# Kernel tuning notes

Measured on AMD Instinct MI355X. Metric: run time of the kernel, lower is better.

## Reference

```python
import jax, jax.numpy as jnp
import numpy as np

EMBED_DIM = 1024
NUM_HEADS = 16
HEAD_DIM = EMBED_DIM // NUM_HEADS
SEG_LEN = 1024  # all segment_lengths equal, dilation_rate == 1


def setup_inputs() -> dict:
    key = jax.random.key(0)
    k1, k2, k3 = jax.random.split(key, 3)
    B, S, E = 2, 4096, EMBED_DIM
    x = jax.random.normal(k1, (B, S, E), dtype=jnp.float32)
    w_qkv = jax.random.normal(k2, (3 * E, E), dtype=jnp.float32) * (E ** -0.5)
    b_qkv = jnp.zeros((3 * E,), dtype=jnp.float32)
    w_out = jax.random.normal(k3, (E, E), dtype=jnp.float32) * (E ** -0.5)
    b_out = jnp.zeros((E,), dtype=jnp.float32)
    return {"x": x, "w_qkv": w_qkv, "b_qkv": b_qkv, "w_out": w_out, "b_out": b_out}


def reference(x, w_qkv, b_qkv, w_out, b_out):
    B, S, E = x.shape
    H, Dh = NUM_HEADS, HEAD_DIM
    scale = 1.0 / np.sqrt(Dh).astype(np.float32)
    # QKV projection
    qkv = x @ w_qkv.T + b_qkv                      # [B, S, 3E]
    qkv = qkv.reshape(B, S, 3, H, Dh).transpose(2, 0, 3, 1, 4)  # [3, B, H, S, Dh]
    q, k, v = qkv[0], qkv[1], qkv[2]
    # Segments tile the sequence; each query attends only within its segment
    # (block-diagonal attention; online-softmax combine across segments is
    # trivial since the segments are disjoint in the query dimension).
    n = S // SEG_LEN
    q = q.reshape(B, H, n, SEG_LEN, Dh)
    k = k.reshape(B, H, n, SEG_LEN, Dh)
    v = v.reshape(B, H, n, SEG_LEN, Dh)
    scores = jnp.einsum("bhnqd,bhnkd->bhnqk", q, k) * scale
    attn = jax.nn.softmax(scores, axis=-1)
    out = jnp.einsum("bhnqk,bhnkd->bhnqd", attn, v)  # [B, H, n, seg, Dh]
    out = out.reshape(B, H, S, Dh).transpose(0, 2, 1, 3).reshape(B, S, E)
    return out @ w_out.T + b_out
```

## Files before the change

kernel.cpp:

```cpp
#include <hip/hip_runtime.h>

typedef __bf16 bf16x8 __attribute__((ext_vector_type(8)));
typedef float f32x4 __attribute__((ext_vector_type(4)));

#define SL2E 0.18033688011112042f

__device__ __forceinline__ unsigned short f2bf(float f) {
  union { float f; unsigned u; } v; v.f = f;
  unsigned r = v.u + 0x7fffu + ((v.u >> 16) & 1u);
  return (unsigned short)(r >> 16);
}

__device__ __forceinline__ float fast_exp2(float x) {
#if __has_builtin(__builtin_amdgcn_exp2f)
  return __builtin_amdgcn_exp2f(x);
#else
  return exp2f(x);
#endif
}

__device__ __forceinline__ unsigned pack_bf2(float lo, float hi) {
  union { float f; unsigned u; } a, b;
  a.f = lo; b.f = hi;
#if __has_builtin(__builtin_amdgcn_perm)
  return __builtin_amdgcn_perm(b.u + 0x7fffu, a.u + 0x7fffu, 0x07060302u);
#else
  return ((b.u + 0x7fffu) & 0xffff0000u) | ((a.u + 0x7fffu) >> 16);
#endif
}

__global__ void f32_to_bf16_k(const float* __restrict__ in, unsigned short* __restrict__ out, int n4) {
  int i = blockIdx.x * blockDim.x + threadIdx.x;
  if (i >= n4) return;
  float4 v = ((const float4*)in)[i];
  ushort4 o;
  o.x = f2bf(v.x); o.y = f2bf(v.y); o.z = f2bf(v.z); o.w = f2bf(v.w);
  ((ushort4*)out)[i] = o;
}

__global__ __launch_bounds__(256) void gemm_qkv(
    const unsigned short* __restrict__ A,
    const unsigned short* __restrict__ Bt,
    const float* __restrict__ bias,
    unsigned short* __restrict__ Qb,
    unsigned short* __restrict__ Kb,
    unsigned short* __restrict__ Vtb) {
  const int K = 1024;
  __shared__ unsigned short As[128 * 40];
  __shared__ unsigned short Bs[128 * 40];
  int tid = threadIdx.x;
  int m0 = blockIdx.x * 128, n0 = blockIdx.y * 128;
  int w = tid >> 6, lane = tid & 63, l15 = lane & 15, quad = lane >> 4;
  int wm = (w & 1) * 64, wn = (w >> 1) * 64;

  f32x4 acc[4][4] = {};

  int c0 = tid, c1 = tid + 256;
  int ra0 = c0 >> 2, ca0 = (c0 & 3) * 8;
  int ra1 = c1 >> 2, ca1 = (c1 & 3) * 8;

  for (int kt = 0; kt < K; kt += 32) {
    __syncthreads();
    uint4 a0 = *(const uint4*)(A + (m0 + ra0) * K + kt + ca0);
    uint4 a1 = *(const uint4*)(A + (m0 + ra1) * K + kt + ca1);
    uint4 b0 = *(const uint4*)(Bt + (n0 + ra0) * K + kt + ca0);
    uint4 b1 = *(const uint4*)(Bt + (n0 + ra1) * K + kt + ca1);
    *(uint4*)(As + ra0 * 40 + ca0) = a0;
    *(uint4*)(As + ra1 * 40 + ca1) = a1;
    *(uint4*)(Bs + ra0 * 40 + ca0) = b0;
    *(uint4*)(Bs + ra1 * 40 + ca1) = b1;
    __syncthreads();
    bf16x8 af[4], bfr[4];
#pragma unroll
    for (int i = 0; i < 4; ++i) af[i] = *(const bf16x8*)(As + (wm + i * 16 + l15) * 40 + quad * 8);
#pragma unroll
    for (int j = 0; j < 4; ++j) bfr[j] = *(const bf16x8*)(Bs + (wn + j * 16 + l15) * 40 + quad * 8);
#pragma unroll
    for (int i = 0; i < 4; ++i)
#pragma unroll
      for (int j = 0; j < 4; ++j)
        acc[i][j] = __builtin_amdgcn_mfma_f32_16x16x32_bf16(af[i], bfr[j], acc[i][j], 0, 0, 0);
  }

  int b = m0 >> 12;
  int sblk = (m0 & 4095) + wm + quad * 4;
#pragma unroll
  for (int j = 0; j < 4; ++j) {
    int n_j = n0 + wn + j * 16 + l15;
    float bv = bias[n_j];
    int t = n_j >> 10, h = (n_j >> 6) & 15, d = n_j & 63;
    if (t == 2) {
      int vbase = ((b * 16 + h) * 64 + d) * 4096;
#pragma unroll
      for (int i = 0; i < 4; ++i) {
        int s = sblk + i * 16;
        ushort4 pk;
        pk.x = f2bf(acc[i][j][0] + bv);
        pk.y = f2bf(acc[i][j][1] + bv);
        pk.z = f2bf(acc[i][j][2] + bv);
        pk.w = f2bf(acc[i][j][3] + bv);
        *(ushort4*)(Vtb + vbase + s) = pk;
      }
    } else {
      unsigned short* dst = (t == 0) ? Qb : Kb;
      float sc = (t == 0) ? SL2E : 1.0f;
      int base = (b * 16 + h) * 4096 * 64 + d;
#pragma unroll
      for (int i = 0; i < 4; ++i)
#pragma unroll
        for (int r = 0; r < 4; ++r) {
          int s = sblk + i * 16 + r;
          dst[base + s * 64] = f2bf((acc[i][j][r] + bv) * sc);
        }
    }
  }
}

#define LDP 72

__global__ __launch_bounds__(256) void attn_k(
    const unsigned short* __restrict__ Qb,
    const unsigned short* __restrict__ Kb,
    const unsigned short* __restrict__ Vtb,
    unsigned short* __restrict__ Ab) {
  __shared__ unsigned short Ks[64 * LDP];
  __shared__ unsigned short Vs[64 * LDP];
  __shared__ unsigned short Ps[4][64 * LDP];

  int tid = threadIdx.x;
  int idx = blockIdx.x;
  int qblk = idx & 3, seg = (idx >> 2) & 3, h = (idx >> 4) & 15, b = idx >> 8;
  int w = tid >> 6, lane = tid & 63, l15 = lane & 15, quad = lane >> 4;
  int bh = b * 16 + h;
  int q0 = seg * 1024 + qblk * 256 + w * 64;

  const unsigned short* Qg = Qb + (bh * 4096 + q0) * 64;
  bf16x8 qf[4][2];
#pragma unroll
  for (int qb = 0; qb < 4; ++qb)
#pragma unroll
    for (int kk = 0; kk < 2; ++kk)
      qf[qb][kk] = *(const bf16x8*)(Qg + (qb * 16 + l15) * 64 + kk * 32 + quad * 8);

  bf16x8 ones;
#pragma unroll
  for (int i = 0; i < 8; ++i) ones[i] = (__bf16)1.0f;

  f32x4 o[4][4] = {};
  f32x4 lacc[4] = {};
  unsigned short* Pw = Ps[w];

  int sr = tid >> 3;
  int sc = (tid & 7) * 8;
  const unsigned short* Kg = Kb + (bh * 4096 + seg * 1024) * 64;
  const unsigned short* Vg = Vtb + bh * 64 * 4096 + seg * 1024;

  for (int kt = 0; kt < 16; ++kt) {
    int s0 = kt * 64;
    __syncthreads();
    *(uint4*)(Ks + sr * LDP + sc)        = *(const uint4*)(Kg + (s0 + sr) * 64 + sc);
    *(uint4*)(Ks + (sr + 32) * LDP + sc) = *(const uint4*)(Kg + (s0 + sr + 32) * 64 + sc);
    *(uint4*)(Vs + sr * LDP + sc)        = *(const uint4*)(Vg + sr * 4096 + s0 + sc);
    *(uint4*)(Vs + (sr + 32) * LDP + sc) = *(const uint4*)(Vg + (sr + 32) * 4096 + s0 + sc);
    __syncthreads();

#pragma unroll
    for (int half = 0; half < 2; ++half) {
      f32x4 st[2][4] = {};
#pragma unroll
      for (int kk = 0; kk < 2; ++kk) {
        bf16x8 kf0 = *(const bf16x8*)(Ks + (half * 32 + l15) * LDP + kk * 32 + quad * 8);
        bf16x8 kf1 = *(const bf16x8*)(Ks + (half * 32 + 16 + l15) * LDP + kk * 32 + quad * 8);
#pragma unroll
        for (int qb = 0; qb < 4; ++qb) {
          st[0][qb] = __builtin_amdgcn_mfma_f32_16x16x32_bf16(kf0, qf[qb][kk], st[0][qb], 0, 0, 0);
          st[1][qb] = __builtin_amdgcn_mfma_f32_16x16x32_bf16(kf1, qf[qb][kk], st[1][qb], 0, 0, 0);
        }
      }
#pragma unroll
      for (int kb = 0; kb < 2; ++kb)
#pragma unroll
        for (int qb = 0; qb < 4; ++qb) {
          f32x4 s = st[kb][qb];
          float p0 = fast_exp2(s[0]), p1 = fast_exp2(s[1]);
          float p2 = fast_exp2(s[2]), p3 = fast_exp2(s[3]);
          uint2 d;
          d.x = pack_bf2(p0, p1);
          d.y = pack_bf2(p2, p3);
          *(uint2*)(Pw + (qb * 16 + l15) * LDP + (half * 2 + kb) * 16 + quad * 4) = d;
        }
    }

#pragma unroll
    for (int kk = 0; kk < 2; ++kk) {
      bf16x8 vf[4];
#pragma unroll
      for (int db = 0; db < 4; ++db)
        vf[db] = *(const bf16x8*)(Vs + (db * 16 + l15) * LDP + kk * 32 + quad * 8);
#pragma unroll
      for (int qb = 0; qb < 4; ++qb) {
        bf16x8 pf = *(const bf16x8*)(Pw + (qb * 16 + l15) * LDP + kk * 32 + quad * 8);
        lacc[qb] = __builtin_amdgcn_mfma_f32_16x16x32_bf16(pf, ones, lacc[qb], 0, 0, 0);
#pragma unroll
        for (int db = 0; db < 4; ++db)
          o[qb][db] = __builtin_amdgcn_mfma_f32_16x16x32_bf16(pf, vf[db], o[qb][db], 0, 0, 0);
      }
    }
  }

#pragma unroll
  for (int qb = 0; qb < 4; ++qb)
#pragma unroll
    for (int r = 0; r < 4; ++r) {
      float inv = 1.0f / lacc[qb][r];
      int sg = q0 + qb * 16 + quad * 4 + r;
      int base = (b * 4096 + sg) * 1024 + h * 64;
#pragma unroll
      for (int db = 0; db < 4; ++db)
        Ab[base + db * 16 + l15] = f2bf(o[qb][db][r] * inv);
    }
}

__global__ __launch_bounds__(256) void gemm_out(
    const unsigned short* __restrict__ A,
    const unsigned short* __restrict__ Bt,
    const float* __restrict__ bias,
    float* __restrict__ C) {
  const int K = 1024;
  __shared__ unsigned short As[128 * 40];
  __shared__ unsigned short Bs[128 * 40];
  int tid = threadIdx.x;
  int m0 = blockIdx.x * 128, n0 = blockIdx.y * 128;
  int w = tid >> 6, lane = tid & 63, l15 = lane & 15, quad = lane >> 4;
  int wm = (w & 1) * 64, wn = (w >> 1) * 64;

  f32x4 acc[4][4] = {};

  int c0 = tid, c1 = tid + 256;
  int ra0 = c0 >> 2, ca0 = (c0 & 3) * 8;
  int ra1 = c1 >> 2, ca1 = (c1 & 3) * 8;

  for (int kt = 0; kt < K; kt += 32) {
    __syncthreads();
    uint4 a0 = *(const uint4*)(A + (m0 + ra0) * K + kt + ca0);
    uint4 a1 = *(const uint4*)(A + (m0 + ra1) * K + kt + ca1);
    uint4 b0 = *(const uint4*)(Bt + (n0 + ra0) * K + kt + ca0);
    uint4 b1 = *(const uint4*)(Bt + (n0 + ra1) * K + kt + ca1);
    *(uint4*)(As + ra0 * 40 + ca0) = a0;
    *(uint4*)(As + ra1 * 40 + ca1) = a1;
    *(uint4*)(Bs + ra0 * 40 + ca0) = b0;
    *(uint4*)(Bs + ra1 * 40 + ca1) = b1;
    __syncthreads();
    bf16x8 af[4], bfr[4];
#pragma unroll
    for (int i = 0; i < 4; ++i) af[i] = *(const bf16x8*)(As + (wm + i * 16 + l15) * 40 + quad * 8);
#pragma unroll
    for (int j = 0; j < 4; ++j) bfr[j] = *(const bf16x8*)(Bs + (wn + j * 16 + l15) * 40 + quad * 8);
#pragma unroll
    for (int i = 0; i < 4; ++i)
#pragma unroll
      for (int j = 0; j < 4; ++j)
        acc[i][j] = __builtin_amdgcn_mfma_f32_16x16x32_bf16(af[i], bfr[j], acc[i][j], 0, 0, 0);
  }

#pragma unroll
  for (int j = 0; j < 4; ++j) {
    int n_j = n0 + wn + j * 16 + l15;
    float bv = bias[n_j];
#pragma unroll
    for (int i = 0; i < 4; ++i)
#pragma unroll
      for (int r = 0; r < 4; ++r) {
        int m = m0 + wm + i * 16 + quad * 4 + r;
        C[m * 1024 + n_j] = acc[i][j][r] + bv;
      }
  }
}

extern "C" void kernel_launch(void* const* d_in, const int* in_sizes, int n_in,
                              void* d_out, int out_size, void* d_ws, size_t ws_size,
                              hipStream_t stream) {
  const float* x     = (const float*)d_in[0];
  const float* w_qkv = (const float*)d_in[1];
  const float* b_qkv = (const float*)d_in[2];
  const float* w_out = (const float*)d_in[3];
  const float* b_out = (const float*)d_in[4];
  float* out = (float*)d_out;
  char* ws = (char*)d_ws;

  unsigned short* wqkvb = (unsigned short*)(ws);
  unsigned short* woutb = (unsigned short*)(ws + 6291456);
  unsigned short* Qb    = (unsigned short*)(ws + 8388608);
  unsigned short* Kb    = (unsigned short*)(ws + 25165824);
  unsigned short* Vtb   = (unsigned short*)(ws + 41943040);
  unsigned short* xb    = (unsigned short*)(ws + 58720256);
  unsigned short* Ab    = xb;

  f32_to_bf16_k<<<8192, 256, 0, stream>>>(x, xb, 2097152);
  f32_to_bf16_k<<<3072, 256, 0, stream>>>(w_qkv, wqkvb, 786432);
  f32_to_bf16_k<<<1024, 256, 0, stream>>>(w_out, woutb, 262144);
  gemm_qkv<<<dim3(64, 24), 256, 0, stream>>>(xb, wqkvb, b_qkv, Qb, Kb, Vtb);
  attn_k<<<512, 256, 0, stream>>>(Qb, Kb, Vtb, Ab);
  gemm_out<<<dim3(64, 8), 256, 0, stream>>>(Ab, woutb, b_out, out);
}
```

Before: 266.8 us.

## Use direct global-to-LDS loads in GEMMs, shrink attention P buffer, fuse conversions

Merges the three fp32-to-bf16 conversion launches into one kernel. Both GEMMs now stage A/B tiles with global_load_lds straight into unpadded 32-wide LDS rows, skipping the register round trip. The attention kernel replaces the MFMA-with-ones row-sum with a scalar accumulation plus cross-lane shuffles. It also shrinks each wave's P staging buffer to 16 rows, written per query block, with a launch-bounds hint of 3 blocks per CU for higher occupancy. Risks are LDS bank conflicts from the unpadded layout and a row sum taken from fp32 probabilities rather than the bf16-rounded ones fed to the PV MFMA.

```diff
diff --git a/kernel.cpp b/kernel.cpp
--- a/kernel.cpp
+++ b/kernel.cpp
@@ -29,13 +29,25 @@
 #endif
 }
 
-__global__ void f32_to_bf16_k(const float* __restrict__ in, unsigned short* __restrict__ out, int n4) {
-  int i = blockIdx.x * blockDim.x + threadIdx.x;
-  if (i >= n4) return;
-  float4 v = ((const float4*)in)[i];
+__device__ __forceinline__ void gload16(const unsigned short* g, unsigned short* l) {
+  __builtin_amdgcn_global_load_lds(
+      (const __attribute__((address_space(1))) unsigned int*)g,
+      (__attribute__((address_space(3))) unsigned int*)l, 16, 0, 0);
+}
+
+__global__ __launch_bounds__(256) void f32_to_bf16_all(
+    const float* __restrict__ x, const float* __restrict__ wq, const float* __restrict__ wo,
+    unsigned short* __restrict__ xb, unsigned short* __restrict__ wqb, unsigned short* __restrict__ wob) {
+  int i = blockIdx.x * 256 + threadIdx.x;
+  const float* src; unsigned short* dst; int off;
+  if (i < 2097152) { src = x; dst = xb; off = i; }
+  else if (i < 2883584) { src = wq; dst = wqb; off = i - 2097152; }
+  else if (i < 3145728) { src = wo; dst = wob; off = i - 2883584; }
+  else return;
+  float4 v = ((const float4*)src)[off];
   ushort4 o;
   o.x = f2bf(v.x); o.y = f2bf(v.y); o.z = f2bf(v.z); o.w = f2bf(v.w);
-  ((ushort4*)out)[i] = o;
+  ((ushort4*)dst)[off] = o;
 }
 
 __global__ __launch_bounds__(256) void gemm_qkv(
@@ -46,8 +58,8 @@
     unsigned short* __restrict__ Kb,
     unsigned short* __restrict__ Vtb) {
   const int K = 1024;
-  __shared__ unsigned short As[128 * 40];
-  __shared__ unsigned short Bs[128 * 40];
+  __shared__ unsigned short As[128 * 32];
+  __shared__ unsigned short Bs[128 * 32];
   int tid = threadIdx.x;
   int m0 = blockIdx.x * 128, n0 = blockIdx.y * 128;
   int w = tid >> 6, lane = tid & 63, l15 = lane & 15, quad = lane >> 4;
@@ -55,26 +67,24 @@
 
   f32x4 acc[4][4] = {};
 
-  int c0 = tid, c1 = tid + 256;
-  int ra0 = c0 >> 2, ca0 = (c0 & 3) * 8;
-  int ra1 = c1 >> 2, ca1 = (c1 & 3) * 8;
+  int srow = lane >> 2, scol = (lane & 3) * 8;
+  const unsigned short* Ag0 = A + (m0 + w * 32 + srow) * K + scol;
+  const unsigned short* Bg0 = Bt + (n0 + w * 32 + srow) * K + scol;
+  unsigned short* Asl = As + w * 1024 + lane * 8;
+  unsigned short* Bsl = Bs + w * 1024 + lane * 8;
 
   for (int kt = 0; kt < K; kt += 32) {
     __syncthreads();
-    uint4 a0 = *(const uint4*)(A + (m0 + ra0) * K + kt + ca0);
-    uint4 a1 = *(const uint4*)(A + (m0 + ra1) * K + kt + ca1);
-    uint4 b0 = *(const uint4*)(Bt + (n0 + ra0) * K + kt + ca0);
-    uint4 b1 = *(const uint4*)(Bt + (n0 + ra1) * K + kt + ca1);
-    *(uint4*)(As + ra0 * 40 + ca0) = a0;
-    *(uint4*)(As + ra1 * 40 + ca1) = a1;
-    *(uint4*)(Bs + ra0 * 40 + ca0) = b0;
-    *(uint4*)(Bs + ra1 * 40 + ca1) = b1;
+    gload16(Ag0 + kt, Asl);
+    gload16(Ag0 + 16 * K + kt, Asl + 512);
+    gload16(Bg0 + kt, Bsl);
+    gload16(Bg0 + 16 * K + kt, Bsl + 512);
     __syncthreads();
     bf16x8 af[4], bfr[4];
 #pragma unroll
-    for (int i = 0; i < 4; ++i) af[i] = *(const bf16x8*)(As + (wm + i * 16 + l15) * 40 + quad * 8);
-#pragma unroll
-    for (int j = 0; j < 4; ++j) bfr[j] = *(const bf16x8*)(Bs + (wn + j * 16 + l15) * 40 + quad * 8);
+    for (int i = 0; i < 4; ++i) af[i] = *(const bf16x8*)(As + (wm + i * 16 + l15) * 32 + quad * 8);
+#pragma unroll
+    for (int j = 0; j < 4; ++j) bfr[j] = *(const bf16x8*)(Bs + (wn + j * 16 + l15) * 32 + quad * 8);
 #pragma unroll
     for (int i = 0; i < 4; ++i)
 #pragma unroll
@@ -118,14 +128,14 @@
 
 #define LDP 72
 
-__global__ __launch_bounds__(256) void attn_k(
+__global__ __launch_bounds__(256, 3) void attn_k(
     const unsigned short* __restrict__ Qb,
     const unsigned short* __restrict__ Kb,
     const unsigned short* __restrict__ Vtb,
     unsigned short* __restrict__ Ab) {
   __shared__ unsigned short Ks[64 * LDP];
   __shared__ unsigned short Vs[64 * LDP];
-  __shared__ unsigned short Ps[4][64 * LDP];
+  __shared__ unsigned short Ps[4][16 * LDP];
 
   int tid = threadIdx.x;
   int idx = blockIdx.x;
@@ -142,12 +152,8 @@
     for (int kk = 0; kk < 2; ++kk)
       qf[qb][kk] = *(const bf16x8*)(Qg + (qb * 16 + l15) * 64 + kk * 32 + quad * 8);
 
-  bf16x8 ones;
-#pragma unroll
-  for (int i = 0; i < 8; ++i) ones[i] = (__bf16)1.0f;
-
   f32x4 o[4][4] = {};
-  f32x4 lacc[4] = {};
+  float lsum[4] = {0.f, 0.f, 0.f, 0.f};
   unsigned short* Pw = Ps[w];
 
   int sr = tid >> 3;
@@ -164,6 +170,7 @@
     *(uint4*)(Vs + (sr + 32) * LDP + sc) = *(const uint4*)(Vg + (sr + 32) * 4096 + s0 + sc);
     __syncthreads();
 
+    uint2 pp[4][4];
 #pragma unroll
     for (int half = 0; half < 2; ++half) {
       f32x4 st[2][4] = {};
@@ -184,35 +191,50 @@
           f32x4 s = st[kb][qb];
           float p0 = fast_exp2(s[0]), p1 = fast_exp2(s[1]);
           float p2 = fast_exp2(s[2]), p3 = fast_exp2(s[3]);
+          lsum[qb] += (p0 + p1) + (p2 + p3);
           uint2 d;
           d.x = pack_bf2(p0, p1);
           d.y = pack_bf2(p2, p3);
-          *(uint2*)(Pw + (qb * 16 + l15) * LDP + (half * 2 + kb) * 16 + quad * 4) = d;
+          pp[qb][half * 2 + kb] = d;
         }
     }
 
-#pragma unroll
-    for (int kk = 0; kk < 2; ++kk) {
-      bf16x8 vf[4];
+    bf16x8 vf[2][4];
+#pragma unroll
+    for (int kk = 0; kk < 2; ++kk)
 #pragma unroll
       for (int db = 0; db < 4; ++db)
-        vf[db] = *(const bf16x8*)(Vs + (db * 16 + l15) * LDP + kk * 32 + quad * 8);
-#pragma unroll
-      for (int qb = 0; qb < 4; ++qb) {
-        bf16x8 pf = *(const bf16x8*)(Pw + (qb * 16 + l15) * LDP + kk * 32 + quad * 8);
-        lacc[qb] = __builtin_amdgcn_mfma_f32_16x16x32_bf16(pf, ones, lacc[qb], 0, 0, 0);
+        vf[kk][db] = *(const bf16x8*)(Vs + (db * 16 + l15) * LDP + kk * 32 + quad * 8);
+#pragma unroll
+    for (int qb = 0; qb < 4; ++qb) {
+#pragma unroll
+      for (int g = 0; g < 4; ++g)
+        *(uint2*)(Pw + l15 * LDP + g * 16 + quad * 4) = pp[qb][g];
+#pragma unroll
+      for (int kk = 0; kk < 2; ++kk) {
+        bf16x8 pa = *(const bf16x8*)(Pw + l15 * LDP + kk * 32 + quad * 8);
 #pragma unroll
         for (int db = 0; db < 4; ++db)
-          o[qb][db] = __builtin_amdgcn_mfma_f32_16x16x32_bf16(pf, vf[db], o[qb][db], 0, 0, 0);
+          o[qb][db] = __builtin_amdgcn_mfma_f32_16x16x32_bf16(pa, vf[kk][db], o[qb][db], 0, 0, 0);
       }
     }
   }
 
 #pragma unroll
+  for (int qb = 0; qb < 4; ++qb) {
+    lsum[qb] += __shfl_xor(lsum[qb], 16);
+    lsum[qb] += __shfl_xor(lsum[qb], 32);
+  }
+  float* Pf = (float*)Ps[w];
+  if (quad == 0) {
+#pragma unroll
+    for (int qb = 0; qb < 4; ++qb) Pf[qb * 16 + l15] = lsum[qb];
+  }
+#pragma unroll
   for (int qb = 0; qb < 4; ++qb)
 #pragma unroll
     for (int r = 0; r < 4; ++r) {
-      float inv = 1.0f / lacc[qb][r];
+      float inv = 1.0f / Pf[qb * 16 + quad * 4 + r];
       int sg = q0 + qb * 16 + quad * 4 + r;
       int base = (b * 4096 + sg) * 1024 + h * 64;
 #pragma unroll
@@ -227,8 +249,8 @@
     const float* __restrict__ bias,
     float* __restrict__ C) {
   const int K = 1024;
-  __shared__ unsigned short As[128 * 40];
-  __shared__ unsigned short Bs[128 * 40];
+  __shared__ unsigned short As[128 * 32];
+  __shared__ unsigned short Bs[128 * 32];
   int tid = threadIdx.x;
   int m0 = blockIdx.x * 128, n0 = blockIdx.y * 128;
   int w = tid >> 6, lane = tid & 63, l15 = lane & 15, quad = lane >> 4;
@@ -236,26 +258,24 @@
 
   f32x4 acc[4][4] = {};
 
-  int c0 = tid, c1 = tid + 256;
-  int ra0 = c0 >> 2, ca0 = (c0 & 3) * 8;
-  int ra1 = c1 >> 2, ca1 = (c1 & 3) * 8;
+  int srow = lane >> 2, scol = (lane & 3) * 8;
+  const unsigned short* Ag0 = A + (m0 + w * 32 + srow) * K + scol;
+  const unsigned short* Bg0 = Bt + (n0 + w * 32 + srow) * K + scol;
+  unsigned short* Asl = As + w * 1024 + lane * 8;
+  unsigned short* Bsl = Bs + w * 1024 + lane * 8;
 
   for (int kt = 0; kt < K; kt += 32) {
     __syncthreads();
-    uint4 a0 = *(const uint4*)(A + (m0 + ra0) * K + kt + ca0);
-    uint4 a1 = *(const uint4*)(A + (m0 + ra1) * K + kt + ca1);
-    uint4 b0 = *(const uint4*)(Bt + (n0 + ra0) * K + kt + ca0);
-    uint4 b1 = *(const uint4*)(Bt + (n0 + ra1) * K + kt + ca1);
-    *(uint4*)(As + ra0 * 40 + ca0) = a0;
-    *(uint4*)(As + ra1 * 40 + ca1) = a1;
-    *(uint4*)(Bs + ra0 * 40 + ca0) = b0;
-    *(uint4*)(Bs + ra1 * 40 + ca1) = b1;
+    gload16(Ag0 + kt, Asl);
+    gload16(Ag0 + 16 * K + kt, Asl + 512);
+    gload16(Bg0 + kt, Bsl);
+    gload16(Bg0 + 16 * K + kt, Bsl + 512);
     __syncthreads();
     bf16x8 af[4], bfr[4];
 #pragma unroll
-    for (int i = 0; i < 4; ++i) af[i] = *(const bf16x8*)(As + (wm + i * 16 + l15) * 40 + quad * 8);
-#pragma unroll
-    for (int j = 0; j < 4; ++j) bfr[j] = *(const bf16x8*)(Bs + (wn + j * 16 + l15) * 40 + quad * 8);
+    for (int i = 0; i < 4; ++i) af[i] = *(const bf16x8*)(As + (wm + i * 16 + l15) * 32 + quad * 8);
+#pragma unroll
+    for (int j = 0; j < 4; ++j) bfr[j] = *(const bf16x8*)(Bs + (wn + j * 16 + l15) * 32 + quad * 8);
 #pragma unroll
     for (int i = 0; i < 4; ++i)
 #pragma unroll
@@ -296,9 +316,7 @@
   unsigned short* xb    = (unsigned short*)(ws + 58720256);
   unsigned short* Ab    = xb;
 
-  f32_to_bf16_k<<<8192, 256, 0, stream>>>(x, xb, 2097152);
-  f32_to_bf16_k<<<3072, 256, 0, stream>>>(w_qkv, wqkvb, 786432);
-  f32_to_bf16_k<<<1024, 256, 0, stream>>>(w_out, woutb, 262144);
+  f32_to_bf16_all<<<12288, 256, 0, stream>>>(x, w_qkv, w_out, xb, wqkvb, woutb);
   gemm_qkv<<<dim3(64, 24), 256, 0, stream>>>(xb, wqkvb, b_qkv, Qb, Kb, Vtb);
   attn_k<<<512, 256, 0, stream>>>(Qb, Kb, Vtb, Ab);
   gemm_out<<<dim3(64, 8), 256, 0, stream>>>(Ab, woutb, b_out, out);
```

Result: slower. 305.9 us (+14.7%).

## Double-buffer attention K/V via direct LDS loads, fuse conversions, vectorize output

Applied to the files above, without the earlier changes.

The attention kernel now prefetches the next K/V tile with global_load_lds into a double-buffered, XOR-swizzled LDS area. This overlaps loads with MFMA work and drops one barrier per iteration. Row sums are accumulated in registers instead of through an extra MFMA against a ones vector, and P is staged through a smaller per-wave LDS buffer one 16-row block at a time. The output is transposed through LDS so it can be written as 16-byte vector stores. Block ordering is remapped, and the three f32-to-bf16 conversion launches are merged into one kernel. The risks are summing the un-rounded fp32 probabilities rather than the bf16 values, and the correctness of the swizzled global_load_lds layout.

```diff
diff --git a/kernel.cpp b/kernel.cpp
--- a/kernel.cpp
+++ b/kernel.cpp
@@ -29,13 +29,25 @@
 #endif
 }
 
-__global__ void f32_to_bf16_k(const float* __restrict__ in, unsigned short* __restrict__ out, int n4) {
-  int i = blockIdx.x * blockDim.x + threadIdx.x;
-  if (i >= n4) return;
-  float4 v = ((const float4*)in)[i];
+__device__ __forceinline__ void gload16(const unsigned short* g, unsigned short* l) {
+  __builtin_amdgcn_global_load_lds(
+      (const __attribute__((address_space(1))) unsigned int*)g,
+      (__attribute__((address_space(3))) unsigned int*)l, 16, 0, 0);
+}
+
+__global__ __launch_bounds__(256) void f32_to_bf16_all(
+    const float* __restrict__ x, const float* __restrict__ wq, const float* __restrict__ wo,
+    unsigned short* __restrict__ xb, unsigned short* __restrict__ wqb, unsigned short* __restrict__ wob) {
+  int i = blockIdx.x * 256 + threadIdx.x;
+  const float* src; unsigned short* dst; int off;
+  if (i < 2097152) { src = x; dst = xb; off = i; }
+  else if (i < 2883584) { src = wq; dst = wqb; off = i - 2097152; }
+  else if (i < 3145728) { src = wo; dst = wob; off = i - 2883584; }
+  else return;
+  float4 v = ((const float4*)src)[off];
   ushort4 o;
   o.x = f2bf(v.x); o.y = f2bf(v.y); o.z = f2bf(v.z); o.w = f2bf(v.w);
-  ((ushort4*)out)[i] = o;
+  ((ushort4*)dst)[off] = o;
 }
 
 __global__ __launch_bounds__(256) void gemm_qkv(
@@ -118,22 +130,30 @@
 
 #define LDP 72
 
+#define SWZ(r, cg) ((((r) * 8) + ((cg) ^ ((r) & 7))) * 8)
+
 __global__ __launch_bounds__(256) void attn_k(
     const unsigned short* __restrict__ Qb,
     const unsigned short* __restrict__ Kb,
     const unsigned short* __restrict__ Vtb,
     unsigned short* __restrict__ Ab) {
-  __shared__ unsigned short Ks[64 * LDP];
-  __shared__ unsigned short Vs[64 * LDP];
-  __shared__ unsigned short Ps[4][64 * LDP];
+  __shared__ unsigned short KV[2][2][4096];
+  __shared__ unsigned short Ps[4][16 * LDP];
 
   int tid = threadIdx.x;
   int idx = blockIdx.x;
-  int qblk = idx & 3, seg = (idx >> 2) & 3, h = (idx >> 4) & 15, b = idx >> 8;
+  int grp = idx & 127, qblk = idx >> 7;
+  int seg = grp & 3, h = (grp >> 2) & 15, b = grp >> 6;
   int w = tid >> 6, lane = tid & 63, l15 = lane & 15, quad = lane >> 4;
   int bh = b * 16 + h;
   int q0 = seg * 1024 + qblk * 256 + w * 64;
 
+  const unsigned short* Kg = Kb + (bh * 4096 + seg * 1024) * 64;
+  const unsigned short* Vg = Vtb + bh * 64 * 4096 + seg * 1024;
+
+  int r0 = w * 16 + (lane >> 3);
+  int cs = ((lane & 7) ^ (lane >> 3)) * 8;
+
   const unsigned short* Qg = Qb + (bh * 4096 + q0) * 64;
   bf16x8 qf[4][2];
 #pragma unroll
@@ -142,35 +162,45 @@
     for (int kk = 0; kk < 2; ++kk)
       qf[qb][kk] = *(const bf16x8*)(Qg + (qb * 16 + l15) * 64 + kk * 32 + quad * 8);
 
-  bf16x8 ones;
-#pragma unroll
-  for (int i = 0; i < 8; ++i) ones[i] = (__bf16)1.0f;
-
   f32x4 o[4][4] = {};
-  f32x4 lacc[4] = {};
+  float lsum[4] = {0.f, 0.f, 0.f, 0.f};
   unsigned short* Pw = Ps[w];
 
-  int sr = tid >> 3;
-  int sc = (tid & 7) * 8;
-  const unsigned short* Kg = Kb + (bh * 4096 + seg * 1024) * 64;
-  const unsigned short* Vg = Vtb + bh * 64 * 4096 + seg * 1024;
-
+  {
+    unsigned short* dk = &KV[0][0][w * 1024];
+    unsigned short* dv = &KV[0][1][w * 1024];
+    gload16(Kg + r0 * 64 + cs, dk);
+    gload16(Kg + (r0 + 8) * 64 + cs, dk + 512);
+    gload16(Vg + r0 * 4096 + cs, dv);
+    gload16(Vg + (r0 + 8) * 4096 + cs, dv + 512);
+  }
+
+#pragma unroll 2
   for (int kt = 0; kt < 16; ++kt) {
-    int s0 = kt * 64;
-    __syncthreads();
-    *(uint4*)(Ks + sr * LDP + sc)        = *(const uint4*)(Kg + (s0 + sr) * 64 + sc);
-    *(uint4*)(Ks + (sr + 32) * LDP + sc) = *(const uint4*)(Kg + (s0 + sr + 32) * 64 + sc);
-    *(uint4*)(Vs + sr * LDP + sc)        = *(const uint4*)(Vg + sr * 4096 + s0 + sc);
-    *(uint4*)(Vs + (sr + 32) * LDP + sc) = *(const uint4*)(Vg + (sr + 32) * 4096 + s0 + sc);
-    __syncthreads();
-
+    int cur = kt & 1;
+    __syncthreads();
+    if (kt < 15) {
+      unsigned short* dk = &KV[cur ^ 1][0][w * 1024];
+      unsigned short* dv = &KV[cur ^ 1][1][w * 1024];
+      const unsigned short* kN = Kg + (kt + 1) * 4096;
+      const unsigned short* vN = Vg + (kt + 1) * 64;
+      gload16(kN + r0 * 64 + cs, dk);
+      gload16(kN + (r0 + 8) * 64 + cs, dk + 512);
+      gload16(vN + r0 * 4096 + cs, dv);
+      gload16(vN + (r0 + 8) * 4096 + cs, dv + 512);
+    }
+    const unsigned short* Kt = KV[cur][0];
+    const unsigned short* Vt = KV[cur][1];
+
+    uint2 pp[4][4];
 #pragma unroll
     for (int half = 0; half < 2; ++half) {
       f32x4 st[2][4] = {};
 #pragma unroll
       for (int kk = 0; kk < 2; ++kk) {
-        bf16x8 kf0 = *(const bf16x8*)(Ks + (half * 32 + l15) * LDP + kk * 32 + quad * 8);
-        bf16x8 kf1 = *(const bf16x8*)(Ks + (half * 32 + 16 + l15) * LDP + kk * 32 + quad * 8);
+        int cg = kk * 4 + quad;
+        bf16x8 kf0 = *(const bf16x8*)(Kt + SWZ(half * 32 + l15, cg));
+        bf16x8 kf1 = *(const bf16x8*)(Kt + SWZ(half * 32 + 16 + l15, cg));
 #pragma unroll
         for (int qb = 0; qb < 4; ++qb) {
           st[0][qb] = __builtin_amdgcn_mfma_f32_16x16x32_bf16(kf0, qf[qb][kk], st[0][qb], 0, 0, 0);
@@ -184,41 +214,68 @@
           f32x4 s = st[kb][qb];
           float p0 = fast_exp2(s[0]), p1 = fast_exp2(s[1]);
           float p2 = fast_exp2(s[2]), p3 = fast_exp2(s[3]);
+          lsum[qb] += (p0 + p1) + (p2 + p3);
           uint2 d;
           d.x = pack_bf2(p0, p1);
           d.y = pack_bf2(p2, p3);
-          *(uint2*)(Pw + (qb * 16 + l15) * LDP + (half * 2 + kb) * 16 + quad * 4) = d;
+          pp[qb][half * 2 + kb] = d;
         }
     }
 
-#pragma unroll
-    for (int kk = 0; kk < 2; ++kk) {
-      bf16x8 vf[4];
+    bf16x8 vf[2][4];
+#pragma unroll
+    for (int kk = 0; kk < 2; ++kk)
 #pragma unroll
       for (int db = 0; db < 4; ++db)
-        vf[db] = *(const bf16x8*)(Vs + (db * 16 + l15) * LDP + kk * 32 + quad * 8);
-#pragma unroll
-      for (int qb = 0; qb < 4; ++qb) {
-        bf16x8 pf = *(const bf16x8*)(Pw + (qb * 16 + l15) * LDP + kk * 32 + quad * 8);
-        lacc[qb] = __builtin_amdgcn_mfma_f32_16x16x32_bf16(pf, ones, lacc[qb], 0, 0, 0);
+        vf[kk][db] = *(const bf16x8*)(Vt + SWZ(db * 16 + l15, kk * 4 + quad));
+#pragma unroll
+    for (int qb = 0; qb < 4; ++qb) {
+#pragma unroll
+      for (int g = 0; g < 4; ++g)
+        *(uint2*)(Pw + l15 * LDP + g * 16 + quad * 4) = pp[qb][g];
+#pragma unroll
+      for (int kk = 0; kk < 2; ++kk) {
+        bf16x8 pa = *(const bf16x8*)(Pw + l15 * LDP + kk * 32 + quad * 8);
 #pragma unroll
         for (int db = 0; db < 4; ++db)
-          o[qb][db] = __builtin_amdgcn_mfma_f32_16x16x32_bf16(pf, vf[db], o[qb][db], 0, 0, 0);
+          o[qb][db] = __builtin_amdgcn_mfma_f32_16x16x32_bf16(pa, vf[kk][db], o[qb][db], 0, 0, 0);
       }
     }
   }
 
 #pragma unroll
-  for (int qb = 0; qb < 4; ++qb)
-#pragma unroll
-    for (int r = 0; r < 4; ++r) {
-      float inv = 1.0f / lacc[qb][r];
-      int sg = q0 + qb * 16 + quad * 4 + r;
-      int base = (b * 4096 + sg) * 1024 + h * 64;
-#pragma unroll
-      for (int db = 0; db < 4; ++db)
-        Ab[base + db * 16 + l15] = f2bf(o[qb][db][r] * inv);
-    }
+  for (int qb = 0; qb < 4; ++qb) {
+    lsum[qb] += __shfl_xor(lsum[qb], 16);
+    lsum[qb] += __shfl_xor(lsum[qb], 32);
+  }
+
+  float* Wf = (float*)(&KV[0][0][0]) + w * 1024;
+#pragma unroll
+  for (int qb = 0; qb < 4; ++qb) {
+#pragma unroll
+    for (int db = 0; db < 4; ++db)
+#pragma unroll
+      for (int r = 0; r < 4; ++r)
+        Wf[(quad * 4 + r) * 64 + db * 16 + l15] = o[qb][db][r];
+    float inv = 1.0f / lsum[qb];
+    float4 x0 = *(float4*)(Wf + l15 * 64 + quad * 8);
+    float4 x1 = *(float4*)(Wf + l15 * 64 + quad * 8 + 4);
+    float4 x2 = *(float4*)(Wf + l15 * 64 + (quad + 4) * 8);
+    float4 x3 = *(float4*)(Wf + l15 * 64 + (quad + 4) * 8 + 4);
+    uint4 u0, u1;
+    u0.x = pack_bf2(x0.x * inv, x0.y * inv);
+    u0.y = pack_bf2(x0.z * inv, x0.w * inv);
+    u0.z = pack_bf2(x1.x * inv, x1.y * inv);
+    u0.w = pack_bf2(x1.z * inv, x1.w * inv);
+    u1.x = pack_bf2(x2.x * inv, x2.y * inv);
+    u1.y = pack_bf2(x2.z * inv, x2.w * inv);
+    u1.z = pack_bf2(x3.x * inv, x3.y * inv);
+    u1.w = pack_bf2(x3.z * inv, x3.w * inv);
+    int sg = q0 + qb * 16 + l15;
+    int base = (b * 4096 + sg) * 1024 + h * 64;
+    *(uint4*)(Ab + base + quad * 8) = u0;
+    *(uint4*)(Ab + base + (quad + 4) * 8) = u1;
+  }
 }
 
 __global__ __launch_bounds__(256) void gemm_out(
@@ -296,9 +353,7 @@
   unsigned short* xb    = (unsigned short*)(ws + 58720256);
   unsigned short* Ab    = xb;
 
-  f32_to_bf16_k<<<8192, 256, 0, stream>>>(x, xb, 2097152);
-  f32_to_bf16_k<<<3072, 256, 0, stream>>>(w_qkv, wqkvb, 786432);
-  f32_to_bf16_k<<<1024, 256, 0, stream>>>(w_out, woutb, 262144);
+  f32_to_bf16_all<<<12288, 256, 0, stream>>>(x, w_qkv, w_out, xb, wqkvb, woutb);
   gemm_qkv<<<dim3(64, 24), 256, 0, stream>>>(xb, wqkvb, b_qkv, Qb, Kb, Vtb);
   attn_k<<<512, 256, 0, stream>>>(Qb, Kb, Vtb, Ab);
   gemm_out<<<dim3(64, 8), 256, 0, stream>>>(Ab, woutb, b_out, out);
```

Measured after the change: 259.8 us. 2.6% less time.
